# Kernel optimization log

Hardware: AMD Instinct MI355X
Metric: run time of the kernel (lower is better)

## Reference

```python
import jax, jax.numpy as jnp
import numpy as np

N_NODES_PER_GRAPH = 200
N_GRAPHS = 32
N = N_NODES_PER_GRAPH * N_GRAPHS        # 6400 nodes
E = N_GRAPHS * N_NODES_PER_GRAPH ** 2   # 1.28M edges
IN_DIM = 200
HID = 32
HEADS = 1
N_CLASSES = 2
BN_EPS = 1e-5


def setup_inputs() -> dict:
    key = jax.random.key(0)
    ks = jax.random.split(key, 32)
    p = lambda k, shape: (jax.random.normal(k, shape, dtype=jnp.float32) * 0.1)
    inp = {
        'x': jax.random.normal(ks[0], (N, IN_DIM), dtype=jnp.float32),
        'edge_attr': jax.random.normal(ks[1], (E,), dtype=jnp.float32),
        'edge_index': jax.random.randint(ks[2], (2, E), 0, N),
        'batch': jax.random.randint(ks[3], (N,), 0, N_GRAPHS),
        # ---- GAT block 1 (in=200 -> hid=32) ----
        'w1': p(ks[4], (IN_DIM, HEADS * HID)),
        'asrc1': p(ks[5], (HEADS, HID)),
        'adst1': p(ks[6], (HEADS, HID)),
        'b1': p(ks[7], (HEADS * HID,)),
        'elw1': p(ks[8], (2 * HID + 1, HID)),   # edge_lin for edge_node_concate
        'elb1': p(ks[9], (HID,)),
        'pw1': p(ks[10], (HEADS * HID, HID)),   # block projection Linear
        'pb1': p(ks[11], (HID,)),
        'bng1': 1.0 + p(ks[12], (HID,)),
        'bnb1': p(ks[13], (HID,)),
        # ---- GAT block 2 (in=32 -> hid=32, proj=final_node_dim=32) ----
        'w2': p(ks[14], (HID, HEADS * HID)),
        'asrc2': p(ks[15], (HEADS, HID)),
        'adst2': p(ks[16], (HEADS, HID)),
        'b2': p(ks[17], (HEADS * HID,)),
        'elw2': p(ks[18], (2 * HID + 1, HID)),
        'elb2': p(ks[19], (HID,)),
        'pw2': p(ks[20], (HEADS * HID, HID)),
        'pb2': p(ks[21], (HID,)),
        'bng2': 1.0 + p(ks[22], (HID,)),
        'bnb2': p(ks[23], (HID,)),
        # ---- classifier head (BasicMLP as single Linear) ----
        'fw': p(ks[24], (HID, N_CLASSES)),
        'fb': p(ks[25], (N_CLASSES,)),
    }
    return inp


def _gat_block(x, src, dst, ew_abs, W, asrc, adst, b, elw, elb, pw, pb, bng, bnb):
    """MPGATConv(edge_node_concate) + Linear + LeakyReLU + BatchNorm1d(eval)."""
    n = x.shape[0]
    H, C = asrc.shape
    xp = (x @ W).reshape(n, H, C)                       # [N,H,C] per-head projection
    al_s = jnp.sum(xp * asrc, axis=-1)                  # [N,H] alpha_src
    al_d = jnp.sum(xp * adst, axis=-1)                  # [N,H] alpha_dst
    a = jax.nn.leaky_relu(al_s[src] + al_d[dst], 0.2)   # [E,H]
    # scatter-softmax over destination index
    m = jax.ops.segment_max(a, dst, num_segments=n)
    m = jnp.where(jnp.isfinite(m), m, 0.0)
    e = jnp.exp(a - m[dst])
    s = jax.ops.segment_sum(e, dst, num_segments=n)
    alpha = e / jnp.where(s[dst] == 0, 1.0, s[dst])     # [E,H]
    # message: concat(x_i, x_j * alpha, |edge_w|) -> edge_lin
    ewb = jnp.broadcast_to(ew_abs[:, None, None], (ew_abs.shape[0], H, 1))
    msg = jnp.concatenate([xp[dst], xp[src] * alpha[..., None], ewb], axis=-1)
    msg = msg @ elw + elb                               # [E,H,C]
    agg = jax.ops.segment_sum(msg, dst, num_segments=n).reshape(n, H * C) + b
    # block tail: Linear -> LeakyReLU -> BatchNorm1d (eval, running stats 0/1)
    z = jax.nn.leaky_relu(agg @ pw + pb, 0.2)
    z = z * (bng / np.float32(np.sqrt(1.0 + BN_EPS))) + bnb
    return z


def reference(x, edge_attr,
              w1, asrc1, adst1, b1, elw1, elb1, pw1, pb1, bng1, bnb1,
              w2, asrc2, adst2, b2, elw2, elb2, pw2, pb2, bng2, bnb2,
              fw, fb, edge_index, batch):
    src, dst = edge_index[0], edge_index[1]             # j (source), i (target)
    ew = jnp.abs(edge_attr)                             # use_abs_weight=True
    z = _gat_block(x, src, dst, ew, w1, asrc1, adst1, b1, elw1, elb1, pw1, pb1, bng1, bnb1)
    z = _gat_block(z, src, dst, ew, w2, asrc2, adst2, b2, elw2, elb2, pw2, pb2, bng2, bnb2)
    # global mean pool over graphs
    tot = jax.ops.segment_sum(z, batch, num_segments=N_GRAPHS)
    cnt = jax.ops.segment_sum(jnp.ones((z.shape[0],), z.dtype), batch, num_segments=N_GRAPHS)
    g = tot / jnp.maximum(cnt, 1.0)[:, None]            # [B, HID]
    return g @ fw + fb                                  # [B, n_classes]
```

## Files before the change

kernel.cpp:

```cpp
#include <hip/hip_runtime.h>
#include <hip/hip_bf16.h>


#define HID 32
#define NB_SORT 512
#define BUCK_SHIFT 5
#define BUCK_BINS 32
#define NBUCK_MAX 256
#define ECAP 8192
#define DCAP 512

typedef unsigned short ushort_t;
typedef unsigned int uint_t;

__global__ void k_bhist(const int* __restrict__ dst, int* __restrict__ bpart_T,
                        int E, int nbuck, int nb, int chunk) {
    __shared__ int h[NBUCK_MAX];
    for (int i = threadIdx.x; i < nbuck; i += blockDim.x) h[i] = 0;
    __syncthreads();
    int b = blockIdx.x;
    int lo = b * chunk, hi = min(lo + chunk, E);
    for (int e = lo + threadIdx.x; e < hi; e += blockDim.x)
        atomicAdd(&h[dst[e] >> BUCK_SHIFT], 1);
    __syncthreads();
    for (int g = threadIdx.x; g < nbuck; g += blockDim.x)
        bpart_T[(size_t)g * nb + b] = h[g];
}

__global__ void k_bcur(const int* __restrict__ bpart_T, int* __restrict__ bcur_T,
                       int* __restrict__ bcnt, int nb) {
    __shared__ int wsum_[4];
    int g = blockIdx.x;
    const int2* row = (const int2*)(bpart_T + (size_t)g * nb);
    int t = threadIdx.x;
    int2 v = row[t];
    int s = v.x + v.y;
    int lane = t & 63, wid = t >> 6;
    int p = s;
    #pragma unroll
    for (int d = 1; d < 64; d <<= 1) { int u = __shfl_up(p, d); if (lane >= d) p += u; }
    if (lane == 63) wsum_[wid] = p;
    __syncthreads();
    int add = 0;
    for (int i = 0; i < wid; i++) add += wsum_[i];
    int excl = p + add - s;
    int2 w; w.x = excl; w.y = excl + v.x;
    ((int2*)(bcur_T + (size_t)g * nb))[t] = w;
    if (t == blockDim.x - 1) bcnt[g] = excl + s;
}

__global__ void k_bscatter(const int* __restrict__ src, const int* __restrict__ dst,
                           const float* __restrict__ ea, const int* __restrict__ bcur_T,
                           uint2* __restrict__ ebuf, int E, int nbuck, int nb, int chunk) {
    __shared__ int cur[NBUCK_MAX];
    int b = blockIdx.x;
    for (int g = threadIdx.x; g < nbuck; g += blockDim.x)
        cur[g] = (g << 13) + bcur_T[(size_t)g * nb + b];
    __syncthreads();
    int lo = b * chunk, hi = min(lo + chunk, E);
    for (int e = lo + threadIdx.x; e < hi; e += blockDim.x) {
        int d = dst[e];
        int p = atomicAdd(&cur[d >> BUCK_SHIFT], 1);
        uint2 v;
        v.x = ((uint_t)d << 16) | (uint_t)src[e];
        v.y = __float_as_uint(fabsf(ea[e]));
        ebuf[p] = v;
    }
}

__global__ void k_bsort(const uint2* __restrict__ ebuf, const int* __restrict__ bcnt,
                        int* __restrict__ begs, int* __restrict__ ends,
                        float* __restrict__ wsum, ushort_t* __restrict__ ssrc,
                        int nbins, int nbuck) {
    __shared__ int hist[BUCK_BINS];
    __shared__ int cur[BUCK_BINS];
    __shared__ int sexc[BUCK_BINS];
    __shared__ float hw[BUCK_BINS];
    __shared__ ushort_t sbuf[ECAP];
    int g = blockIdx.x;
    if (g >= nbuck) return;
    int binlo = g << BUCK_SHIFT;
    int nbin = min(BUCK_BINS, nbins - binlo);
    int base = g << 13;
    int cnt = bcnt[g];
    int t = threadIdx.x;
    if (t < BUCK_BINS) { hist[t] = 0; hw[t] = 0.f; }
    __syncthreads();
    for (int i = t; i < cnt; i += blockDim.x) {
        uint2 v = ebuf[base + i];
        int dl = (int)(v.x >> 16) - binlo;
        atomicAdd(&hist[dl], 1);
        atomicAdd(&hw[dl], __uint_as_float(v.y));
    }
    __syncthreads();
    if (t < BUCK_BINS) {
        int v = hist[t];
        int p = v;
        #pragma unroll
        for (int d = 1; d < 32; d <<= 1) { int u = __shfl_up(p, d); if (t >= d) p += u; }
        cur[t] = p - v;
        sexc[t] = p - v;
    }
    __syncthreads();
    if (t < nbin) {
        begs[binlo + t] = base + sexc[t];
        ends[binlo + t] = base + sexc[t] + hist[t];
        wsum[binlo + t] = hw[t];
    }
    if (cnt <= ECAP) {
        for (int i = t; i < cnt; i += blockDim.x) {
            uint_t v = ebuf[base + i].x;
            int dl = (int)(v >> 16) - binlo;
            int p = atomicAdd(&cur[dl], 1);
            sbuf[p] = (ushort_t)(v & 0xFFFFu);
        }
        __syncthreads();
        for (int i = t; i < cnt; i += blockDim.x)
            ssrc[base + i] = sbuf[i];
    } else {
        for (int i = t; i < cnt; i += blockDim.x) {
            uint_t v = ebuf[base + i].x;
            int dl = (int)(v >> 16) - binlo;
            int p = atomicAdd(&cur[dl], 1);
            ssrc[base + p] = (ushort_t)(v & 0xFFFFu);
        }
    }
}

__device__ __forceinline__ void node_epilogue(float xp, int r, int l,
        const float* __restrict__ asrc, const float* __restrict__ adst,
        const float* __restrict__ elw,
        float* __restrict__ ys, float* __restrict__ yd,
        float* __restrict__ als, float* __restrict__ ald) {
    float ps = xp * asrc[l], pd = xp * adst[l];
    #pragma unroll
    for (int mask = 16; mask >= 1; mask >>= 1) {
        ps += __shfl_xor(ps, mask);
        pd += __shfl_xor(pd, mask);
    }
    if (l == 0) { als[r] = ps; ald[r] = pd; }
    int gbase = threadIdx.x & 32;
    float yss = 0.f, ydd = 0.f;
    #pragma unroll
    for (int k = 0; k < HID; k++) {
        float xk = __shfl(xp, gbase + k);
        yss = fmaf(xk, elw[(HID + k) * HID + l], yss);
        ydd = fmaf(xk, elw[k * HID + l], ydd);
    }
    ys[r * HID + l] = yss;
    yd[r * HID + l] = ydd;
}

__global__ void k_b1prep(const float* __restrict__ x, const float* __restrict__ w1,
                         const float* __restrict__ asrc, const float* __restrict__ adst,
                         const float* __restrict__ elw,
                         float* __restrict__ ys, float* __restrict__ yd,
                         float* __restrict__ als, float* __restrict__ ald,
                         int n, int K) {
    extern __shared__ float wlds[];
    for (int i = threadIdx.x; i < K * HID; i += blockDim.x) wlds[i] = w1[i];
    __syncthreads();
    int l = threadIdx.x & 31;
    int r = blockIdx.x * (blockDim.x >> 5) + (threadIdx.x >> 5);
    if (r >= n) return;
    const float4* rowv = (const float4*)(x + (size_t)r * K);
    float acc = 0.f;
    for (int k4 = 0; k4 < (K >> 2); k4++) {
        float4 v = rowv[k4];
        int k = k4 << 2;
        acc = fmaf(v.x, wlds[(k + 0) * HID + l], acc);
        acc = fmaf(v.y, wlds[(k + 1) * HID + l], acc);
        acc = fmaf(v.z, wlds[(k + 2) * HID + l], acc);
        acc = fmaf(v.w, wlds[(k + 3) * HID + l], acc);
    }
    node_epilogue(acc, r, l, asrc, adst, elw, ys, yd, als, ald);
}

#define LEAKY(a) ((a) >= 0.f ? (a) : 0.2f * (a))

__device__ __forceinline__ float gat_node_z(int node, int lane,
        float* __restrict__ wbuf, int* __restrict__ jbuf,
        const int* __restrict__ begs, const int* __restrict__ ends,
        const ushort_t* __restrict__ ssrc, const float* __restrict__ wsum,
        const float* __restrict__ als, const float* __restrict__ ald,
        const float* __restrict__ ys, const float* __restrict__ yd,
        const float* __restrict__ elw, const float* __restrict__ elb,
        const float* __restrict__ bvec, const float* __restrict__ pw,
        const float* __restrict__ pb, const float* __restrict__ bng,
        const float* __restrict__ bnb) {
    int beg = begs[node], end = ends[node];
    int deg = end - beg;
    int half = lane >> 5, l = lane & 31;
    float aldi = ald[node];
    float agg;
    if (deg > 0) {
        int degc = min(deg, DCAP);
        float mreg = -INFINITY;
        for (int i = lane; i < deg; i += 64) {
            int j = ssrc[beg + i];
            float a = LEAKY(als[j] + aldi);
            mreg = fmaxf(mreg, a);
            if (i < DCAP) { wbuf[i] = a; jbuf[i] = j; }
        }
        #pragma unroll
        for (int mask = 32; mask >= 1; mask >>= 1)
            mreg = fmaxf(mreg, __shfl_xor(mreg, mask));
        float m = mreg;
        __threadfence_block();
        float es = 0.f;
        for (int i = lane; i < degc; i += 64) {
            float w = __expf(wbuf[i] - m);
            es += w;
            wbuf[i] = w;
        }
        #pragma unroll
        for (int mask = 32; mask >= 1; mask >>= 1)
            es += __shfl_xor(es, mask);
        __threadfence_block();
        int mid = degc >> 1;
        int e = half ? mid : 0;
        int e1 = half ? degc : mid;
        float acc0 = 0.f, acc1 = 0.f;
        for (; e + 8 <= e1; e += 8) {
            int j0 = jbuf[e + 0], j1 = jbuf[e + 1], j2 = jbuf[e + 2], j3 = jbuf[e + 3];
            int j4 = jbuf[e + 4], j5 = jbuf[e + 5], j6 = jbuf[e + 6], j7 = jbuf[e + 7];
            float w0 = wbuf[e + 0], w1 = wbuf[e + 1], w2 = wbuf[e + 2], w3 = wbuf[e + 3];
            float w4 = wbuf[e + 4], w5 = wbuf[e + 5], w6 = wbuf[e + 6], w7 = wbuf[e + 7];
            acc0 = fmaf(w0, ys[j0 * HID + l], acc0);
            acc1 = fmaf(w1, ys[j1 * HID + l], acc1);
            acc0 = fmaf(w2, ys[j2 * HID + l], acc0);
            acc1 = fmaf(w3, ys[j3 * HID + l], acc1);
            acc0 = fmaf(w4, ys[j4 * HID + l], acc0);
            acc1 = fmaf(w5, ys[j5 * HID + l], acc1);
            acc0 = fmaf(w6, ys[j6 * HID + l], acc0);
            acc1 = fmaf(w7, ys[j7 * HID + l], acc1);
        }
        for (; e < e1; e++)
            acc0 = fmaf(wbuf[e], ys[jbuf[e] * HID + l], acc0);
        float esT = 0.f;
        for (int e2 = beg + DCAP + half; e2 < end; e2 += 2) {
            int j = ssrc[e2];
            float w = __expf(LEAKY(als[j] + aldi) - m);
            esT += w;
            acc0 = fmaf(w, ys[j * HID + l], acc0);
        }
        float acc = acc0 + acc1;
        acc += __shfl_xor(acc, 32);
        esT += __shfl_xor(esT, 32);
        agg = acc / (es + esT) + wsum[node] * elw[64 * HID + l];
    } else {
        agg = 0.f;
    }
    agg += (float)deg * (yd[node * HID + l] + elb[l]) + bvec[l];
    float z = 0.f;
    #pragma unroll
    for (int k = 0; k < HID; k++) {
        float av = __shfl(agg, k);
        z = fmaf(av, pw[k * HID + l], z);
    }
    z += pb[l];
    z = LEAKY(z);
    const float inv = 0.99999500003749971875f;
    return fmaf(z, bng[l] * inv, bnb[l]);
}

__global__ void __launch_bounds__(256)
k_gat1(const int* __restrict__ begs, const int* __restrict__ ends,
       const ushort_t* __restrict__ ssrc, const float* __restrict__ wsum,
       const float* __restrict__ als, const float* __restrict__ ald,
       const float* __restrict__ ys, const float* __restrict__ yd,
       const float* __restrict__ elw, const float* __restrict__ elb,
       const float* __restrict__ bvec, const float* __restrict__ pw,
       const float* __restrict__ pb, const float* __restrict__ bng,
       const float* __restrict__ bnb,
       const float* __restrict__ w2, const float* __restrict__ asrc2,
       const float* __restrict__ adst2, const float* __restrict__ elw2,
       float* __restrict__ ys2, float* __restrict__ yd2,
       float* __restrict__ als2, float* __restrict__ ald2, int n) {
    __shared__ float wa[4][DCAP];
    __shared__ int ja[4][DCAP];
    int lane = threadIdx.x & 63;
    int wv = threadIdx.x >> 6;
    int node = blockIdx.x * 4 + wv;
    if (node >= n) return;
    float z = gat_node_z(node, lane, wa[wv], ja[wv], begs, ends, ssrc, wsum,
                         als, ald, ys, yd, elw, elb, bvec, pw, pb, bng, bnb);
    int l = lane & 31, gbase = threadIdx.x & 32;
    float acc = 0.f;
    #pragma unroll
    for (int k = 0; k < HID; k++) {
        float zk = __shfl(z, gbase + k);
        acc = fmaf(zk, w2[k * HID + l], acc);
    }
    node_epilogue(acc, node, l, asrc2, adst2, elw2, ys2, yd2, als2, ald2);
}

__global__ void __launch_bounds__(256)
k_gat2(const int* __restrict__ begs, const int* __restrict__ ends,
       const ushort_t* __restrict__ ssrc, const float* __restrict__ wsum,
       const float* __restrict__ als, const float* __restrict__ ald,
       const float* __restrict__ ys, const float* __restrict__ yd,
       const float* __restrict__ elw, const float* __restrict__ elb,
       const float* __restrict__ bvec, const float* __restrict__ pw,
       const float* __restrict__ pb, const float* __restrict__ bng,
       const float* __restrict__ bnb,
       float* __restrict__ pool, const int* __restrict__ batch, int n) {
    __shared__ float wa[4][DCAP];
    __shared__ int ja[4][DCAP];
    int lane = threadIdx.x & 63;
    int wv = threadIdx.x >> 6;
    int node = blockIdx.x * 4 + wv;
    if (node >= n) return;
    float z = gat_node_z(node, lane, wa[wv], ja[wv], begs, ends, ssrc, wsum,
                         als, ald, ys, yd, elw, elb, bvec, pw, pb, bng, bnb);
    if (lane < 32) atomicAdd(&pool[batch[node] * HID + lane], z);
}

__global__ void k_head(const float* __restrict__ pool, const int* __restrict__ batch,
                       const float* __restrict__ fw, const float* __restrict__ fb,
                       float* __restrict__ out, int n, int ngraphs, int ncls) {
    __shared__ int scnt[64];
    int t = threadIdx.x;
    if (t < ngraphs) scnt[t] = 0;
    __syncthreads();
    for (int i = t; i < n; i += blockDim.x) atomicAdd(&scnt[batch[i]], 1);
    __syncthreads();
    if (t < ngraphs * ncls) {
        int g = t / ncls, c = t % ncls;
        float cc = fmaxf((float)scnt[g], 1.0f);
        float acc = 0.f;
        for (int k = 0; k < HID; k++)
            acc = fmaf(pool[g * HID + k] / cc, fw[k * ncls + c], acc);
        out[t] = acc + fb[c];
    }
}

extern "C" void kernel_launch(void* const* d_in, const int* in_sizes, int n_in,
                              void* d_out, int out_size, void* d_ws, size_t ws_size,
                              hipStream_t stream) {
    const float* x     = (const float*)d_in[0];
    const float* ea    = (const float*)d_in[1];
    const int*   eidx  = (const int*)d_in[2];
    const int*   batch = (const int*)d_in[3];
    const float* w1    = (const float*)d_in[4];
    const float* asrc1 = (const float*)d_in[5];
    const float* adst1 = (const float*)d_in[6];
    const float* b1    = (const float*)d_in[7];
    const float* elw1  = (const float*)d_in[8];
    const float* elb1  = (const float*)d_in[9];
    const float* pw1   = (const float*)d_in[10];
    const float* pb1   = (const float*)d_in[11];
    const float* bng1  = (const float*)d_in[12];
    const float* bnb1  = (const float*)d_in[13];
    const float* w2    = (const float*)d_in[14];
    const float* asrc2 = (const float*)d_in[15];
    const float* adst2 = (const float*)d_in[16];
    const float* b2    = (const float*)d_in[17];
    const float* elw2  = (const float*)d_in[18];
    const float* elb2  = (const float*)d_in[19];
    const float* pw2   = (const float*)d_in[20];
    const float* pb2   = (const float*)d_in[21];
    const float* bng2  = (const float*)d_in[22];
    const float* bnb2  = (const float*)d_in[23];
    const float* fw    = (const float*)d_in[24];
    const float* fb    = (const float*)d_in[25];

    const int E  = in_sizes[1];
    const int N  = in_sizes[3];
    const int K1 = in_sizes[4] / HID;
    const int NCLS = in_sizes[25];
    const int NG = out_size / NCLS;
    const int NBUCK = (N + BUCK_BINS - 1) / BUCK_BINS;

    float* ws = (float*)d_ws;
    size_t off = 0;
    auto alloc = [&](size_t nelem) { size_t r = off; off += nelem; return r; };
    size_t ebuf_off = alloc((size_t)NBUCK * ECAP * 2);
    uint2*    ebuf    = (uint2*)(ws + ebuf_off);
    float*    ys_a    = ws + ebuf_off;
    float*    yd_a    = ws + ebuf_off + (size_t)N * HID;
    float*    ys_b    = ws + ebuf_off + (size_t)N * HID * 2;
    float*    yd_b    = ws + ebuf_off + (size_t)N * HID * 3;
    int*      bpart_T = (int*)(ws + alloc((size_t)NBUCK * NB_SORT));
    int*      bcur_T  = (int*)(ws + alloc((size_t)NBUCK * NB_SORT));
    int*      bcnt    = (int*)(ws + alloc(NBUCK));
    int*      begs    = (int*)(ws + alloc(N));
    int*      ends    = (int*)(ws + alloc(N));
    float*    wsum    = ws + alloc(N);
    ushort_t* ssrc    = (ushort_t*)(ws + alloc(((size_t)NBUCK * ECAP + 1) / 2));
    float*    als_a   = ws + alloc(N);
    float*    ald_a   = ws + alloc(N);
    float*    als_b   = ws + alloc(N);
    float*    ald_b   = ws + alloc(N);
    float*    pool    = ws + alloc((size_t)NG * HID);
    (void)ws_size; (void)n_in;

    const int chunk = (E + NB_SORT - 1) / NB_SORT;

    hipMemsetAsync(pool, 0, NG * HID * sizeof(float), stream);

    k_bhist<<<NB_SORT, 256, 0, stream>>>(eidx + E, bpart_T, E, NBUCK, NB_SORT, chunk);
    k_bcur<<<NBUCK, NB_SORT / 2, 0, stream>>>(bpart_T, bcur_T, bcnt, NB_SORT);
    k_bscatter<<<NB_SORT, 256, 0, stream>>>(eidx, eidx + E, ea, bcur_T, ebuf,
                                            E, NBUCK, NB_SORT, chunk);
    k_bsort<<<NBUCK, 256, 0, stream>>>(ebuf, bcnt, begs, ends, wsum, ssrc, N, NBUCK);

    k_b1prep<<<(N + 7) / 8, 256, K1 * HID * sizeof(float), stream>>>(
        x, w1, asrc1, adst1, elw1, ys_a, yd_a, als_a, ald_a, N, K1);

    k_gat1<<<(N + 3) / 4, 256, 0, stream>>>(begs, ends, ssrc, wsum, als_a, ald_a,
        ys_a, yd_a, elw1, elb1, b1, pw1, pb1, bng1, bnb1,
        w2, asrc2, adst2, elw2, ys_b, yd_b, als_b, ald_b, N);

    k_gat2<<<(N + 3) / 4, 256, 0, stream>>>(begs, ends, ssrc, wsum, als_b, ald_b,
        ys_b, yd_b, elw2, elb2, b2, pw2, pb2, bng2, bnb2, pool, batch, N);

    k_head<<<1, 256, 0, stream>>>(pool, batch, fw, fb, (float*)d_out, N, NG, NCLS);
}
```

Baseline: 112.1 us.

## Store gathered ys features in bf16, pack softmax weights with indices, fuse pool zeroing

The per-node ys feature table that is gathered per edge is now stored in bf16 instead of fp32, halving the bytes moved in the edge aggregation loops. The per-wave LDS buffers for edge weights and source indices are merged into one float2 array, so each edge needs a single LDS load. The separate pool memset is folded into the k_bcur kernel to remove one launch. The bf16 rounding of ys adds precision error to the aggregated messages.

```diff
diff --git a/kernel.cpp b/kernel.cpp
--- a/kernel.cpp
+++ b/kernel.cpp
@@ -13,6 +13,15 @@
 typedef unsigned short ushort_t;
 typedef unsigned int uint_t;
 
+__device__ __forceinline__ ushort_t f2bf(float f) {
+    uint_t u = __float_as_uint(f);
+    u += 0x7FFF + ((u >> 16) & 1);
+    return (ushort_t)(u >> 16);
+}
+__device__ __forceinline__ float bf2f(ushort_t h) {
+    return __uint_as_float(((uint_t)h) << 16);
+}
+
 __global__ void k_bhist(const int* __restrict__ dst, int* __restrict__ bpart_T,
                         int E, int nbuck, int nb, int chunk) {
     __shared__ int h[NBUCK_MAX];
@@ -28,9 +37,12 @@
 }
 
 __global__ void k_bcur(const int* __restrict__ bpart_T, int* __restrict__ bcur_T,
-                       int* __restrict__ bcnt, int nb) {
+                       int* __restrict__ bcnt, float* __restrict__ pool,
+                       int nb, int poolN) {
     __shared__ int wsum_[4];
     int g = blockIdx.x;
+    if (g == 0)
+        for (int i = threadIdx.x; i < poolN; i += blockDim.x) pool[i] = 0.f;
     const int2* row = (const int2*)(bpart_T + (size_t)g * nb);
     int t = threadIdx.x;
     int2 v = row[t];
@@ -130,7 +142,7 @@
 __device__ __forceinline__ void node_epilogue(float xp, int r, int l,
         const float* __restrict__ asrc, const float* __restrict__ adst,
         const float* __restrict__ elw,
-        float* __restrict__ ys, float* __restrict__ yd,
+        ushort_t* __restrict__ ys, float* __restrict__ yd,
         float* __restrict__ als, float* __restrict__ ald) {
     float ps = xp * asrc[l], pd = xp * adst[l];
     #pragma unroll
@@ -147,14 +159,14 @@
         yss = fmaf(xk, elw[(HID + k) * HID + l], yss);
         ydd = fmaf(xk, elw[k * HID + l], ydd);
     }
-    ys[r * HID + l] = yss;
+    ys[r * HID + l] = f2bf(yss);
     yd[r * HID + l] = ydd;
 }
 
 __global__ void k_b1prep(const float* __restrict__ x, const float* __restrict__ w1,
                          const float* __restrict__ asrc, const float* __restrict__ adst,
                          const float* __restrict__ elw,
-                         float* __restrict__ ys, float* __restrict__ yd,
+                         ushort_t* __restrict__ ys, float* __restrict__ yd,
                          float* __restrict__ als, float* __restrict__ ald,
                          int n, int K) {
     extern __shared__ float wlds[];
@@ -179,11 +191,11 @@
 #define LEAKY(a) ((a) >= 0.f ? (a) : 0.2f * (a))
 
 __device__ __forceinline__ float gat_node_z(int node, int lane,
-        float* __restrict__ wbuf, int* __restrict__ jbuf,
+        float2* __restrict__ pbuf,
         const int* __restrict__ begs, const int* __restrict__ ends,
         const ushort_t* __restrict__ ssrc, const float* __restrict__ wsum,
         const float* __restrict__ als, const float* __restrict__ ald,
-        const float* __restrict__ ys, const float* __restrict__ yd,
+        const ushort_t* __restrict__ ys, const float* __restrict__ yd,
         const float* __restrict__ elw, const float* __restrict__ elb,
         const float* __restrict__ bvec, const float* __restrict__ pw,
         const float* __restrict__ pb, const float* __restrict__ bng,
@@ -200,7 +212,7 @@
             int j = ssrc[beg + i];
             float a = LEAKY(als[j] + aldi);
             mreg = fmaxf(mreg, a);
-            if (i < DCAP) { wbuf[i] = a; jbuf[i] = j; }
+            if (i < DCAP) { float2 p; p.x = a; p.y = __int_as_float(j); pbuf[i] = p; }
         }
         #pragma unroll
         for (int mask = 32; mask >= 1; mask >>= 1)
@@ -209,9 +221,9 @@
         __threadfence_block();
         float es = 0.f;
         for (int i = lane; i < degc; i += 64) {
-            float w = __expf(wbuf[i] - m);
+            float w = __expf(pbuf[i].x - m);
             es += w;
-            wbuf[i] = w;
+            pbuf[i].x = w;
         }
         #pragma unroll
         for (int mask = 32; mask >= 1; mask >>= 1)
@@ -222,27 +234,27 @@
         int e1 = half ? degc : mid;
         float acc0 = 0.f, acc1 = 0.f;
         for (; e + 8 <= e1; e += 8) {
-            int j0 = jbuf[e + 0], j1 = jbuf[e + 1], j2 = jbuf[e + 2], j3 = jbuf[e + 3];
-            int j4 = jbuf[e + 4], j5 = jbuf[e + 5], j6 = jbuf[e + 6], j7 = jbuf[e + 7];
-            float w0 = wbuf[e + 0], w1 = wbuf[e + 1], w2 = wbuf[e + 2], w3 = wbuf[e + 3];
-            float w4 = wbuf[e + 4], w5 = wbuf[e + 5], w6 = wbuf[e + 6], w7 = wbuf[e + 7];
-            acc0 = fmaf(w0, ys[j0 * HID + l], acc0);
-            acc1 = fmaf(w1, ys[j1 * HID + l], acc1);
-            acc0 = fmaf(w2, ys[j2 * HID + l], acc0);
-            acc1 = fmaf(w3, ys[j3 * HID + l], acc1);
-            acc0 = fmaf(w4, ys[j4 * HID + l], acc0);
-            acc1 = fmaf(w5, ys[j5 * HID + l], acc1);
-            acc0 = fmaf(w6, ys[j6 * HID + l], acc0);
-            acc1 = fmaf(w7, ys[j7 * HID + l], acc1);
-        }
-        for (; e < e1; e++)
-            acc0 = fmaf(wbuf[e], ys[jbuf[e] * HID + l], acc0);
+            float2 p0 = pbuf[e + 0], p1 = pbuf[e + 1], p2 = pbuf[e + 2], p3 = pbuf[e + 3];
+            float2 p4 = pbuf[e + 4], p5 = pbuf[e + 5], p6 = pbuf[e + 6], p7 = pbuf[e + 7];
+            acc0 = fmaf(p0.x, bf2f(ys[__float_as_int(p0.y) * HID + l]), acc0);
+            acc1 = fmaf(p1.x, bf2f(ys[__float_as_int(p1.y) * HID + l]), acc1);
+            acc0 = fmaf(p2.x, bf2f(ys[__float_as_int(p2.y) * HID + l]), acc0);
+            acc1 = fmaf(p3.x, bf2f(ys[__float_as_int(p3.y) * HID + l]), acc1);
+            acc0 = fmaf(p4.x, bf2f(ys[__float_as_int(p4.y) * HID + l]), acc0);
+            acc1 = fmaf(p5.x, bf2f(ys[__float_as_int(p5.y) * HID + l]), acc1);
+            acc0 = fmaf(p6.x, bf2f(ys[__float_as_int(p6.y) * HID + l]), acc0);
+            acc1 = fmaf(p7.x, bf2f(ys[__float_as_int(p7.y) * HID + l]), acc1);
+        }
+        for (; e < e1; e++) {
+            float2 p = pbuf[e];
+            acc0 = fmaf(p.x, bf2f(ys[__float_as_int(p.y) * HID + l]), acc0);
+        }
         float esT = 0.f;
         for (int e2 = beg + DCAP + half; e2 < end; e2 += 2) {
             int j = ssrc[e2];
             float w = __expf(LEAKY(als[j] + aldi) - m);
             esT += w;
-            acc0 = fmaf(w, ys[j * HID + l], acc0);
+            acc0 = fmaf(w, bf2f(ys[j * HID + l]), acc0);
         }
         float acc = acc0 + acc1;
         acc += __shfl_xor(acc, 32);
@@ -268,22 +280,21 @@
 k_gat1(const int* __restrict__ begs, const int* __restrict__ ends,
        const ushort_t* __restrict__ ssrc, const float* __restrict__ wsum,
        const float* __restrict__ als, const float* __restrict__ ald,
-       const float* __restrict__ ys, const float* __restrict__ yd,
+       const ushort_t* __restrict__ ys, const float* __restrict__ yd,
        const float* __restrict__ elw, const float* __restrict__ elb,
        const float* __restrict__ bvec, const float* __restrict__ pw,
        const float* __restrict__ pb, const float* __restrict__ bng,
        const float* __restrict__ bnb,
        const float* __restrict__ w2, const float* __restrict__ asrc2,
        const float* __restrict__ adst2, const float* __restrict__ elw2,
-       float* __restrict__ ys2, float* __restrict__ yd2,
+       ushort_t* __restrict__ ys2, float* __restrict__ yd2,
        float* __restrict__ als2, float* __restrict__ ald2, int n) {
-    __shared__ float wa[4][DCAP];
-    __shared__ int ja[4][DCAP];
+    __shared__ float2 pa[4][DCAP];
     int lane = threadIdx.x & 63;
     int wv = threadIdx.x >> 6;
     int node = blockIdx.x * 4 + wv;
     if (node >= n) return;
-    float z = gat_node_z(node, lane, wa[wv], ja[wv], begs, ends, ssrc, wsum,
+    float z = gat_node_z(node, lane, pa[wv], begs, ends, ssrc, wsum,
                          als, ald, ys, yd, elw, elb, bvec, pw, pb, bng, bnb);
     int l = lane & 31, gbase = threadIdx.x & 32;
     float acc = 0.f;
@@ -299,19 +310,18 @@
 k_gat2(const int* __restrict__ begs, const int* __restrict__ ends,
        const ushort_t* __restrict__ ssrc, const float* __restrict__ wsum,
        const float* __restrict__ als, const float* __restrict__ ald,
-       const float* __restrict__ ys, const float* __restrict__ yd,
+       const ushort_t* __restrict__ ys, const float* __restrict__ yd,
        const float* __restrict__ elw, const float* __restrict__ elb,
        const float* __restrict__ bvec, const float* __restrict__ pw,
        const float* __restrict__ pb, const float* __restrict__ bng,
        const float* __restrict__ bnb,
        float* __restrict__ pool, const int* __restrict__ batch, int n) {
-    __shared__ float wa[4][DCAP];
-    __shared__ int ja[4][DCAP];
+    __shared__ float2 pa[4][DCAP];
     int lane = threadIdx.x & 63;
     int wv = threadIdx.x >> 6;
     int node = blockIdx.x * 4 + wv;
     if (node >= n) return;
-    float z = gat_node_z(node, lane, wa[wv], ja[wv], begs, ends, ssrc, wsum,
+    float z = gat_node_z(node, lane, pa[wv], begs, ends, ssrc, wsum,
                          als, ald, ys, yd, elw, elb, bvec, pw, pb, bng, bnb);
     if (lane < 32) atomicAdd(&pool[batch[node] * HID + lane], z);
 }
@@ -377,10 +387,10 @@
     auto alloc = [&](size_t nelem) { size_t r = off; off += nelem; return r; };
     size_t ebuf_off = alloc((size_t)NBUCK * ECAP * 2);
     uint2*    ebuf    = (uint2*)(ws + ebuf_off);
-    float*    ys_a    = ws + ebuf_off;
+    ushort_t* ys_a    = (ushort_t*)(ws + ebuf_off);
+    ushort_t* ys_b    = (ushort_t*)(ws + ebuf_off) + (size_t)N * HID;
     float*    yd_a    = ws + ebuf_off + (size_t)N * HID;
-    float*    ys_b    = ws + ebuf_off + (size_t)N * HID * 2;
-    float*    yd_b    = ws + ebuf_off + (size_t)N * HID * 3;
+    float*    yd_b    = ws + ebuf_off + (size_t)N * HID * 2;
     int*      bpart_T = (int*)(ws + alloc((size_t)NBUCK * NB_SORT));
     int*      bcur_T  = (int*)(ws + alloc((size_t)NBUCK * NB_SORT));
     int*      bcnt    = (int*)(ws + alloc(NBUCK));
@@ -397,10 +407,9 @@
 
     const int chunk = (E + NB_SORT - 1) / NB_SORT;
 
-    hipMemsetAsync(pool, 0, NG * HID * sizeof(float), stream);
-
     k_bhist<<<NB_SORT, 256, 0, stream>>>(eidx + E, bpart_T, E, NBUCK, NB_SORT, chunk);
-    k_bcur<<<NBUCK, NB_SORT / 2, 0, stream>>>(bpart_T, bcur_T, bcnt, NB_SORT);
+    k_bcur<<<NBUCK, NB_SORT / 2, 0, stream>>>(bpart_T, bcur_T, bcnt, pool,
+                                              NB_SORT, NG * HID);
     k_bscatter<<<NB_SORT, 256, 0, stream>>>(eidx, eidx + E, ea, bcur_T, ebuf,
                                             E, NBUCK, NB_SORT, chunk);
     k_bsort<<<NBUCK, 256, 0, stream>>>(ebuf, bcnt, begs, ends, wsum, ssrc, N, NBUCK);
```

Result: faster. 107.6 us, median of 2 (-4.0%).
